# Performance work log

Measured on AMD Instinct MI355X. Metric: run time of the kernel, lower is better.

Reference implementation:

```python
import jax, jax.numpy as jnp
import numpy as np

DIM = 1024
N_HEADS = 16
HEAD_DIM = DIM // N_HEADS
EPS = 1e-05
ROPE_BASE = 1000000.0


def apply_rope(x, base=ROPE_BASE):
    # x: [b, seq, heads, head_dim]
    b, seq, n_heads, dim = x.shape
    half = dim // 2
    i = jnp.arange(half)
    theta = 1.0 / base ** (2 * i / dim)
    pos = jnp.arange(seq)
    angles = pos[:, None] * theta[None, :]            # [seq, half]
    cos = jnp.cos(angles)[None, :, None, :]           # [1, seq, 1, half]
    sin = jnp.sin(angles)[None, :, None, :]
    x1, x2 = jnp.split(x, 2, axis=-1)
    return jnp.concatenate([x1 * cos - x2 * sin, x1 * sin + x2 * cos], axis=-1)


def setup_inputs() -> dict:
    key = jax.random.key(0)
    ks = jax.random.split(key, 6)
    b, seq = 2, 2048
    scale = 1.0 / np.sqrt(DIM)
    x = jax.random.normal(ks[0], (b, seq, DIM), dtype=jnp.float32)
    w_norm = jnp.ones((DIM,), dtype=jnp.float32)
    Wq = jax.random.normal(ks[1], (DIM, DIM), dtype=jnp.float32) * scale
    Wk = jax.random.normal(ks[2], (DIM, DIM), dtype=jnp.float32) * scale
    Wv = jax.random.normal(ks[3], (DIM, DIM), dtype=jnp.float32) * scale
    Wo = jax.random.normal(ks[4], (DIM, DIM), dtype=jnp.float32) * scale
    return {"x": x, "w_norm": w_norm, "Wq": Wq, "Wk": Wk, "Wv": Wv, "Wo": Wo}


def reference(x, w_norm, Wq, Wk, Wv, Wo):
    b, seq, d = x.shape
    # RMSNorm
    rms = jnp.sqrt(jnp.mean(x * x, axis=-1, keepdims=True) + EPS)
    x_norm = x / rms * w_norm
    # QKV projections (Dense without bias: y = x @ W)
    q = (x_norm @ Wq).reshape(b, seq, N_HEADS, HEAD_DIM)
    k = (x_norm @ Wk).reshape(b, seq, N_HEADS, HEAD_DIM)
    v = (x_norm @ Wv).reshape(b, seq, N_HEADS, HEAD_DIM)
    q = apply_rope(q)
    k = apply_rope(k)
    # Causal attention with full [b,h,t,s] scores (faithful to source)
    scores = jnp.einsum('bthd,bshd->bhts', q, k) / jnp.sqrt(jnp.float32(HEAD_DIM))
    causal = jnp.triu(jnp.full((seq, seq), -jnp.inf, dtype=scores.dtype), k=1)
    scores = scores + causal[None, None, :, :]
    attn = jax.nn.softmax(scores, axis=-1)
    out = jnp.einsum('bhts,bshd->bthd', attn, v).reshape(b, seq, d)
    return out @ Wo
```

## Files before the change

kernel.cpp:

```cpp
#include <hip/hip_runtime.h>

#define DIM 1024
#define SEQ 2048
#define BATCH 2
#define NHEADS 16
#define HD 64
#define ROWS (BATCH * SEQ)

typedef __bf16 bf16x8 __attribute__((ext_vector_type(8)));
typedef __bf16 bf16x4 __attribute__((ext_vector_type(4)));
typedef float f32x4 __attribute__((ext_vector_type(4)));

__device__ __forceinline__ f32x4 f4zero() {
    f32x4 z = {0.f, 0.f, 0.f, 0.f};
    return z;
}

#define GLOAD_LDS16(g, l)                                                                  \
    __builtin_amdgcn_global_load_lds((const __attribute__((address_space(1))) void*)(g),   \
                                     (__attribute__((address_space(3))) void*)(l), 16, 0, 0)

__global__ __launch_bounds__(256) void rmsnorm_bf16(const float* __restrict__ x,
                                                    const float* __restrict__ w,
                                                    __bf16* __restrict__ xn) {
    int row = blockIdx.x;
    int t = threadIdx.x;
    float4 v = ((const float4*)(x + (size_t)row * DIM))[t];
    float ss = v.x * v.x + v.y * v.y + v.z * v.z + v.w * v.w;
#pragma unroll
    for (int off = 1; off < 64; off <<= 1) ss += __shfl_xor(ss, off);
    __shared__ float red[4];
    if ((t & 63) == 0) red[t >> 6] = ss;
    __syncthreads();
    ss = red[0] + red[1] + red[2] + red[3];
    float scale = rsqrtf(ss * (1.0f / DIM) + 1e-5f);
    float4 wv = ((const float4*)w)[t];
    bf16x4 o;
    o[0] = (__bf16)(v.x * scale * wv.x);
    o[1] = (__bf16)(v.y * scale * wv.y);
    o[2] = (__bf16)(v.z * scale * wv.z);
    o[3] = (__bf16)(v.w * scale * wv.w);
    *(bf16x4*)(xn + (size_t)row * DIM + t * 4) = o;
}

__global__ __launch_bounds__(256) void wcvt_kernel(const float* __restrict__ Wq,
                                                   const float* __restrict__ Wk,
                                                   const float* __restrict__ Wv,
                                                   const float* __restrict__ Wo,
                                                   __bf16* tq, __bf16* tk, __bf16* tv, __bf16* to_) {
    int z = blockIdx.z;
    const float* W = z == 0 ? Wq : z == 1 ? Wk : z == 2 ? Wv : Wo;
    __bf16* T = z == 0 ? tq : z == 1 ? tk : z == 2 ? tv : to_;
    __shared__ float tile[32][33];
    int n0 = blockIdx.x * 32, k0 = blockIdx.y * 32;
    int tx = threadIdx.x & 31, ty = threadIdx.x >> 5;
#pragma unroll
    for (int j = 0; j < 32; j += 8) tile[ty + j][tx] = W[(size_t)(k0 + ty + j) * DIM + n0 + tx];
    __syncthreads();
#pragma unroll
    for (int j = 0; j < 32; j += 8)
        T[(size_t)(n0 + ty + j) * DIM + k0 + tx] = (__bf16)tile[tx][ty + j];
}

__global__ __launch_bounds__(256) void rope_table_kernel(float* __restrict__ cosT,
                                                         float* __restrict__ sinT) {
    int idx = blockIdx.x * 256 + threadIdx.x;
    int s = idx >> 5, i = idx & 31;
    float e = (2.0f * (float)i) / 64.0f;
    float theta = 1.0f / powf(1000000.0f, e);
    float ang = (float)s * theta;
    cosT[idx] = cosf(ang);
    sinT[idx] = sinf(ang);
}

__global__ __launch_bounds__(256) void rope_apply_bf16(__bf16* __restrict__ q,
                                                       __bf16* __restrict__ k,
                                                       const float* __restrict__ cosT,
                                                       const float* __restrict__ sinT) {
    int idx = blockIdx.x * 256 + threadIdx.x;
    __bf16* t = blockIdx.y ? k : q;
    int row = idx >> 6, rem = idx & 63;
    int head = rem >> 2, i0 = (rem & 3) * 8;
    int s = row & (SEQ - 1);
    size_t base = (size_t)row * DIM + head * HD + i0;
    bf16x8 x1 = *(const bf16x8*)&t[base];
    bf16x8 x2 = *(const bf16x8*)&t[base + 32];
    const float* cp = cosT + s * 32 + i0;
    const float* sp = sinT + s * 32 + i0;
    bf16x8 y1, y2;
#pragma unroll
    for (int j = 0; j < 8; ++j) {
        float a = (float)x1[j], b = (float)x2[j];
        float c = cp[j], sn = sp[j];
        y1[j] = (__bf16)(a * c - b * sn);
        y2[j] = (__bf16)(a * sn + b * c);
    }
    *(bf16x8*)&t[base] = y1;
    *(bf16x8*)&t[base + 32] = y2;
}

__global__ __launch_bounds__(256) void vtrans_kernel(const __bf16* __restrict__ v,
                                                     __bf16* __restrict__ vt) {
    __shared__ __bf16 tile[32][33];
    int bh = blockIdx.z;
    int b = bh >> 4, h = bh & 15;
    int s0 = blockIdx.x * 32, d0 = blockIdx.y * 32;
    int tx = threadIdx.x & 31, ty = threadIdx.x >> 5;
    const __bf16* src = v + (size_t)(b * SEQ) * DIM + h * HD;
#pragma unroll
    for (int j = 0; j < 32; j += 8) tile[ty + j][tx] = src[(size_t)(s0 + ty + j) * DIM + d0 + tx];
    __syncthreads();
    __bf16* dst = vt + ((size_t)bh * HD + d0) * SEQ + s0;
#pragma unroll
    for (int j = 0; j < 32; j += 8) dst[(size_t)(ty + j) * SEQ + tx] = tile[tx][ty + j];
}

template <typename OutT>
__device__ __forceinline__ void gemm_body(const __bf16* __restrict__ A,
                                          const __bf16* __restrict__ Bt,
                                          OutT* __restrict__ C,
                                          int K, int N, int row0, int col0) {
    __shared__ __bf16 As[128 * 32];
    __shared__ __bf16 Bs[128 * 32];
    int tid = threadIdx.x;
    int w = tid >> 6, l = tid & 63, l15 = l & 15, g = l >> 4;
    int wr = (w >> 1) << 6, wc = (w & 1) << 6;

    int sr0 = tid >> 2;
    int sr1 = 64 + (tid >> 2);
    int lc0 = (((tid & 3) ^ ((tid >> 3) & 3)) << 3);
    const __bf16* gA0 = A + (size_t)(row0 + sr0) * K + lc0;
    const __bf16* gA1 = A + (size_t)(row0 + sr1) * K + lc0;
    const __bf16* gB0 = Bt + (size_t)(col0 + sr0) * K + lc0;
    const __bf16* gB1 = Bt + (size_t)(col0 + sr1) * K + lc0;
    __bf16* lA0 = As + w * 512;
    __bf16* lA1 = As + 2048 + w * 512;
    __bf16* lB0 = Bs + w * 512;
    __bf16* lB1 = Bs + 2048 + w * 512;

    int rca = ((g ^ ((l15 >> 1) & 3)) << 3);

    f32x4 acc[4][4];
#pragma unroll
    for (int i = 0; i < 4; ++i)
#pragma unroll
        for (int j = 0; j < 4; ++j) acc[i][j] = f4zero();

    for (int k0 = 0; k0 < K; k0 += 32) {
        __syncthreads();
        GLOAD_LDS16(gA0 + k0, lA0);
        GLOAD_LDS16(gA1 + k0, lA1);
        GLOAD_LDS16(gB0 + k0, lB0);
        GLOAD_LDS16(gB1 + k0, lB1);
        __syncthreads();

        bf16x8 af[4], bfr[4];
#pragma unroll
        for (int i = 0; i < 4; ++i) af[i] = *(const bf16x8*)&As[(wr + i * 16 + l15) * 32 + rca];
#pragma unroll
        for (int j = 0; j < 4; ++j) bfr[j] = *(const bf16x8*)&Bs[(wc + j * 16 + l15) * 32 + rca];
        __builtin_amdgcn_s_setprio(1);
#pragma unroll
        for (int i = 0; i < 4; ++i)
#pragma unroll
            for (int j = 0; j < 4; ++j)
                acc[i][j] = __builtin_amdgcn_mfma_f32_16x16x32_bf16(af[i], bfr[j], acc[i][j], 0, 0, 0);
        __builtin_amdgcn_s_setprio(0);
    }
#pragma unroll
    for (int i = 0; i < 4; ++i)
#pragma unroll
        for (int j = 0; j < 4; ++j)
#pragma unroll
            for (int r = 0; r < 4; ++r) {
                int row = row0 + wr + i * 16 + g * 4 + r;
                int col = col0 + wc + j * 16 + l15;
                C[(size_t)row * N + col] = (OutT)acc[i][j][r];
            }
}

__global__ __launch_bounds__(256) void gemm_qkv_kernel(const __bf16* __restrict__ xn,
                                                       const __bf16* __restrict__ wq,
                                                       const __bf16* __restrict__ wk,
                                                       const __bf16* __restrict__ wv,
                                                       __bf16* q, __bf16* k, __bf16* v) {
    int z = blockIdx.z;
    const __bf16* Bt = z == 0 ? wq : z == 1 ? wk : wv;
    __bf16* C = z == 0 ? q : z == 1 ? k : v;
    gemm_body<__bf16>(xn, Bt, C, DIM, DIM, (int)blockIdx.y << 7, (int)blockIdx.x << 7);
}

__global__ __launch_bounds__(256) void gemm_out_kernel(const __bf16* __restrict__ ctx,
                                                       const __bf16* __restrict__ wo,
                                                       float* __restrict__ out) {
    gemm_body<float>(ctx, wo, out, DIM, DIM, (int)blockIdx.y << 7, (int)blockIdx.x << 7);
}

__global__ __launch_bounds__(256) void attn_mfma_kernel(const __bf16* __restrict__ q,
                                                        const __bf16* __restrict__ k,
                                                        const __bf16* __restrict__ vt,
                                                        __bf16* __restrict__ ctx) {
    int bh = blockIdx.x;
    int qt = 31 - (int)blockIdx.y;
    int b = bh >> 4, h = bh & 15;
    int q0 = qt << 6;
    __shared__ __bf16 Ks[128][72];
    __shared__ __bf16 Vl[64][136];
    __shared__ __bf16 Ps[4][16][136];
    int tid = threadIdx.x, w = tid >> 6, l = tid & 63, l15 = l & 15, g = l >> 4;
    size_t hoff = (size_t)(b * SEQ) * DIM + h * HD;
    const __bf16* vth = vt + (size_t)bh * HD * SEQ;

    bf16x8 aq[2];
    {
        int qrow = q0 + w * 16 + l15;
        bf16x8 t0 = *(const bf16x8*)&q[hoff + (size_t)qrow * DIM + g * 8];
        bf16x8 t1 = *(const bf16x8*)&q[hoff + (size_t)qrow * DIM + 32 + g * 8];
        const float c2 = 0.125f * 1.44269504f;
#pragma unroll
        for (int j = 0; j < 8; ++j) {
            aq[0][j] = (__bf16)((float)t0[j] * c2);
            aq[1][j] = (__bf16)((float)t1[j] * c2);
        }
    }

    f32x4 acc_o[4];
#pragma unroll
    for (int j = 0; j < 4; ++j) acc_o[j] = f4zero();
    float m_run[4], l_run[4];
#pragma unroll
    for (int r = 0; r < 4; ++r) {
        m_run[r] = -1e30f;
        l_run[r] = 0.f;
    }

    int ksr = tid >> 3, kd0 = (tid & 7) * 8;
    int vdr = tid >> 4, vs0 = (tid & 15) * 8;

    int nst = (q0 + 191) >> 7;
    bf16x8 rk[4], rv[4];
#pragma unroll
    for (int c = 0; c < 4; ++c) {
        rk[c] = *(const bf16x8*)&k[hoff + (size_t)(c * 32 + ksr) * DIM + kd0];
        rv[c] = *(const bf16x8*)&vth[(size_t)(c * 16 + vdr) * SEQ + vs0];
    }

    for (int st = 0; st < nst; ++st) {
        int s0 = st << 7;
        __syncthreads();
#pragma unroll
        for (int c = 0; c < 4; ++c) {
            *(bf16x8*)&Ks[c * 32 + ksr][kd0] = rk[c];
            *(bf16x8*)&Vl[c * 16 + vdr][vs0] = rv[c];
        }
        __syncthreads();
        if (st + 1 < nst) {
            int sn = s0 + 128;
#pragma unroll
            for (int c = 0; c < 4; ++c) {
                rk[c] = *(const bf16x8*)&k[hoff + (size_t)(sn + c * 32 + ksr) * DIM + kd0];
                rv[c] = *(const bf16x8*)&vth[(size_t)(c * 16 + vdr) * SEQ + sn + vs0];
            }
        }

        f32x4 sacc[8];
#pragma unroll
        for (int j = 0; j < 8; ++j) sacc[j] = f4zero();
        __builtin_amdgcn_s_setprio(1);
#pragma unroll
        for (int j = 0; j < 8; ++j) {
            bf16x8 bk0 = *(const bf16x8*)&Ks[j * 16 + l15][g * 8];
            bf16x8 bk1 = *(const bf16x8*)&Ks[j * 16 + l15][32 + g * 8];
            sacc[j] = __builtin_amdgcn_mfma_f32_16x16x32_bf16(aq[0], bk0, sacc[j], 0, 0, 0);
            sacc[j] = __builtin_amdgcn_mfma_f32_16x16x32_bf16(aq[1], bk1, sacc[j], 0, 0, 0);
        }
        __builtin_amdgcn_s_setprio(0);

        if (st == nst - 1) {
#pragma unroll
            for (int j = 0; j < 8; ++j) {
                int scol = s0 + j * 16 + l15;
#pragma unroll
                for (int r = 0; r < 4; ++r) {
                    int rowq = q0 + w * 16 + g * 4 + r;
                    if (scol > rowq) sacc[j][r] = -1e30f;
                }
            }
        }

#pragma unroll
        for (int r = 0; r < 4; ++r) {
            float tl = sacc[0][r];
#pragma unroll
            for (int j = 1; j < 8; ++j) tl = fmaxf(tl, sacc[j][r]);
            if (!__all(tl <= m_run[r] + 11.0f)) {
#pragma unroll
                for (int off = 1; off < 16; off <<= 1) tl = fmaxf(tl, __shfl_xor(tl, off));
                float m_new = fmaxf(m_run[r], tl);
                float alpha = exp2f(m_run[r] - m_new);
                l_run[r] *= alpha;
#pragma unroll
                for (int jd = 0; jd < 4; ++jd) acc_o[jd][r] *= alpha;
                m_run[r] = m_new;
            }
            float rs = 0.f;
#pragma unroll
            for (int j = 0; j < 8; ++j) {
                float p = exp2f(sacc[j][r] - m_run[r]);
                Ps[w][g * 4 + r][j * 16 + l15] = (__bf16)p;
                rs += p;
            }
#pragma unroll
            for (int off = 1; off < 16; off <<= 1) rs += __shfl_xor(rs, off);
            l_run[r] += rs;
        }

        bf16x8 ap[4];
#pragma unroll
        for (int ks = 0; ks < 4; ++ks) ap[ks] = *(const bf16x8*)&Ps[w][l15][ks * 32 + g * 8];
        __builtin_amdgcn_s_setprio(1);
#pragma unroll
        for (int jd = 0; jd < 4; ++jd)
#pragma unroll
            for (int ks = 0; ks < 4; ++ks) {
                bf16x8 bv = *(const bf16x8*)&Vl[jd * 16 + l15][ks * 32 + g * 8];
                acc_o[jd] = __builtin_amdgcn_mfma_f32_16x16x32_bf16(ap[ks], bv, acc_o[jd], 0, 0, 0);
            }
        __builtin_amdgcn_s_setprio(0);
    }

#pragma unroll
    for (int r = 0; r < 4; ++r) {
        float inv = 1.0f / l_run[r];
        int row = q0 + w * 16 + g * 4 + r;
#pragma unroll
        for (int jd = 0; jd < 4; ++jd)
            ctx[hoff + (size_t)row * DIM + jd * 16 + l15] = (__bf16)(acc_o[jd][r] * inv);
    }
}

extern "C" void kernel_launch(void* const* d_in, const int* in_sizes, int n_in,
                              void* d_out, int out_size, void* d_ws, size_t ws_size,
                              hipStream_t stream) {
    const float* x = (const float*)d_in[0];
    const float* w_norm = (const float*)d_in[1];
    const float* Wq = (const float*)d_in[2];
    const float* Wk = (const float*)d_in[3];
    const float* Wv = (const float*)d_in[4];
    const float* Wo = (const float*)d_in[5];
    float* out = (float*)d_out;
    char* w8 = (char*)d_ws;

    __bf16* xn = (__bf16*)(w8);
    __bf16* wtq = (__bf16*)(w8 + (8ull << 20));
    __bf16* wtk = (__bf16*)(w8 + (10ull << 20));
    __bf16* wtv = (__bf16*)(w8 + (12ull << 20));
    __bf16* wto = (__bf16*)(w8 + (14ull << 20));
    __bf16* qb = (__bf16*)(w8 + (16ull << 20));
    __bf16* kb = (__bf16*)(w8 + (24ull << 20));
    __bf16* vb = (__bf16*)(w8 + (32ull << 20));
    __bf16* vtb = (__bf16*)(w8 + (40ull << 20));
    __bf16* ctx = (__bf16*)(w8 + (48ull << 20));
    float* cosT = (float*)(w8 + (56ull << 20));
    float* sinT = cosT + SEQ * 32;

    wcvt_kernel<<<dim3(32, 32, 4), 256, 0, stream>>>(Wq, Wk, Wv, Wo, wtq, wtk, wtv, wto);
    rmsnorm_bf16<<<ROWS, 256, 0, stream>>>(x, w_norm, xn);
    rope_table_kernel<<<(SEQ * 32) / 256, 256, 0, stream>>>(cosT, sinT);

    gemm_qkv_kernel<<<dim3(DIM / 128, ROWS / 128, 3), 256, 0, stream>>>(xn, wtq, wtk, wtv, qb, kb, vb);

    rope_apply_bf16<<<dim3((ROWS * 64) / 256, 2), 256, 0, stream>>>(qb, kb, cosT, sinT);
    vtrans_kernel<<<dim3(SEQ / 32, HD / 32, BATCH * NHEADS), 256, 0, stream>>>(vb, vtb);

    attn_mfma_kernel<<<dim3(BATCH * NHEADS, SEQ / 64), 256, 0, stream>>>(qb, kb, vtb, ctx);

    gemm_out_kernel<<<dim3(DIM / 128, ROWS / 128), 256, 0, stream>>>(ctx, wto, out);
}
```

Before: 149.5 us.

## Fuse RoPE and V-transpose into QKV GEMM epilogue; rewrite attention with 32x32 MFMA

Applies RoPE in the QKV GEMM epilogue and writes V directly in transposed layout, which removes the separate rope_apply and vtrans kernels along with their global round trips. The attention kernel is rewritten to use 32x32x16 MFMA with 128-query blocks and 64-key tiles. It computes S^T so probabilities stay in registers, repacked with cvt_pk and permlane32_swap instead of going through LDS. The risks are higher register pressure from the two 16-wide accumulators and fewer workgroups in the attention grid.

```diff
diff --git a/kernel.cpp b/kernel.cpp
--- a/kernel.cpp
+++ b/kernel.cpp
@@ -10,10 +10,22 @@
 typedef __bf16 bf16x8 __attribute__((ext_vector_type(8)));
 typedef __bf16 bf16x4 __attribute__((ext_vector_type(4)));
 typedef float f32x4 __attribute__((ext_vector_type(4)));
+typedef float f32x16 __attribute__((ext_vector_type(16)));
+typedef unsigned u32x4 __attribute__((ext_vector_type(4)));
 
 __device__ __forceinline__ f32x4 f4zero() {
     f32x4 z = {0.f, 0.f, 0.f, 0.f};
     return z;
+}
+
+__device__ __forceinline__ unsigned cvtpk(float lo, float hi) {
+    unsigned r;
+    asm("v_cvt_pk_bf16_f32 %0, %1, %2" : "=v"(r) : "v"(lo), "v"(hi));
+    return r;
+}
+
+__device__ __forceinline__ void pl32swap(unsigned& a, unsigned& b) {
+    asm volatile("v_permlane32_swap_b32 %0, %1" : "+v"(a), "+v"(b));
 }
 
 #define GLOAD_LDS16(g, l)                                                                  \
@@ -73,55 +85,10 @@
     sinT[idx] = sinf(ang);
 }
 
-__global__ __launch_bounds__(256) void rope_apply_bf16(__bf16* __restrict__ q,
-                                                       __bf16* __restrict__ k,
-                                                       const float* __restrict__ cosT,
-                                                       const float* __restrict__ sinT) {
-    int idx = blockIdx.x * 256 + threadIdx.x;
-    __bf16* t = blockIdx.y ? k : q;
-    int row = idx >> 6, rem = idx & 63;
-    int head = rem >> 2, i0 = (rem & 3) * 8;
-    int s = row & (SEQ - 1);
-    size_t base = (size_t)row * DIM + head * HD + i0;
-    bf16x8 x1 = *(const bf16x8*)&t[base];
-    bf16x8 x2 = *(const bf16x8*)&t[base + 32];
-    const float* cp = cosT + s * 32 + i0;
-    const float* sp = sinT + s * 32 + i0;
-    bf16x8 y1, y2;
-#pragma unroll
-    for (int j = 0; j < 8; ++j) {
-        float a = (float)x1[j], b = (float)x2[j];
-        float c = cp[j], sn = sp[j];
-        y1[j] = (__bf16)(a * c - b * sn);
-        y2[j] = (__bf16)(a * sn + b * c);
-    }
-    *(bf16x8*)&t[base] = y1;
-    *(bf16x8*)&t[base + 32] = y2;
-}
-
-__global__ __launch_bounds__(256) void vtrans_kernel(const __bf16* __restrict__ v,
-                                                     __bf16* __restrict__ vt) {
-    __shared__ __bf16 tile[32][33];
-    int bh = blockIdx.z;
-    int b = bh >> 4, h = bh & 15;
-    int s0 = blockIdx.x * 32, d0 = blockIdx.y * 32;
-    int tx = threadIdx.x & 31, ty = threadIdx.x >> 5;
-    const __bf16* src = v + (size_t)(b * SEQ) * DIM + h * HD;
-#pragma unroll
-    for (int j = 0; j < 32; j += 8) tile[ty + j][tx] = src[(size_t)(s0 + ty + j) * DIM + d0 + tx];
-    __syncthreads();
-    __bf16* dst = vt + ((size_t)bh * HD + d0) * SEQ + s0;
-#pragma unroll
-    for (int j = 0; j < 32; j += 8) dst[(size_t)(ty + j) * SEQ + tx] = tile[tx][ty + j];
-}
-
-template <typename OutT>
-__device__ __forceinline__ void gemm_body(const __bf16* __restrict__ A,
+__device__ __forceinline__ void gemm_core(const __bf16* __restrict__ A,
                                           const __bf16* __restrict__ Bt,
-                                          OutT* __restrict__ C,
-                                          int K, int N, int row0, int col0) {
-    __shared__ __bf16 As[128 * 32];
-    __shared__ __bf16 Bs[128 * 32];
+                                          int K, __bf16* As, __bf16* Bs,
+                                          f32x4 (&acc)[4][4], int row0, int col0) {
     int tid = threadIdx.x;
     int w = tid >> 6, l = tid & 63, l15 = l & 15, g = l >> 4;
     int wr = (w >> 1) << 6, wc = (w & 1) << 6;
@@ -140,7 +107,6 @@
 
     int rca = ((g ^ ((l15 >> 1) & 3)) << 3);
 
-    f32x4 acc[4][4];
 #pragma unroll
     for (int i = 0; i < 4; ++i)
 #pragma unroll
@@ -167,33 +133,86 @@
                 acc[i][j] = __builtin_amdgcn_mfma_f32_16x16x32_bf16(af[i], bfr[j], acc[i][j], 0, 0, 0);
         __builtin_amdgcn_s_setprio(0);
     }
-#pragma unroll
-    for (int i = 0; i < 4; ++i)
-#pragma unroll
-        for (int j = 0; j < 4; ++j)
-#pragma unroll
-            for (int r = 0; r < 4; ++r) {
-                int row = row0 + wr + i * 16 + g * 4 + r;
-                int col = col0 + wc + j * 16 + l15;
-                C[(size_t)row * N + col] = (OutT)acc[i][j][r];
-            }
 }
 
 __global__ __launch_bounds__(256) void gemm_qkv_kernel(const __bf16* __restrict__ xn,
                                                        const __bf16* __restrict__ wq,
                                                        const __bf16* __restrict__ wk,
                                                        const __bf16* __restrict__ wv,
-                                                       __bf16* q, __bf16* k, __bf16* v) {
+                                                       __bf16* __restrict__ qo,
+                                                       __bf16* __restrict__ ko,
+                                                       __bf16* __restrict__ vt,
+                                                       const float* __restrict__ cosT,
+                                                       const float* __restrict__ sinT) {
+    __shared__ __bf16 As[128 * 32];
+    __shared__ __bf16 Bs[128 * 32];
     int z = blockIdx.z;
     const __bf16* Bt = z == 0 ? wq : z == 1 ? wk : wv;
-    __bf16* C = z == 0 ? q : z == 1 ? k : v;
-    gemm_body<__bf16>(xn, Bt, C, DIM, DIM, (int)blockIdx.y << 7, (int)blockIdx.x << 7);
+    int row0 = (int)blockIdx.y << 7, col0 = (int)blockIdx.x << 7;
+    f32x4 acc[4][4];
+    gemm_core(xn, Bt, DIM, As, Bs, acc, row0, col0);
+
+    int tid = threadIdx.x;
+    int w = tid >> 6, l = tid & 63, l15 = l & 15, g = l >> 4;
+    int wr = (w >> 1) << 6, wc = (w & 1) << 6;
+    int colbase = col0 + wc;
+
+    if (z == 2) {
+        int bh = ((row0 >> 11) << 4) + (colbase >> 6);
+#pragma unroll
+        for (int i = 0; i < 4; ++i) {
+            int sbase = (row0 + wr + i * 16 + g * 4) & (SEQ - 1);
+#pragma unroll
+            for (int j = 0; j < 4; ++j) {
+                int d = j * 16 + l15;
+                bf16x4 o;
+#pragma unroll
+                for (int r = 0; r < 4; ++r) o[r] = (__bf16)acc[i][j][r];
+                *(bf16x4*)&vt[((size_t)bh * HD + d) * SEQ + sbase] = o;
+            }
+        }
+    } else {
+        __bf16* C = z == 0 ? qo : ko;
+#pragma unroll
+        for (int i = 0; i < 4; ++i) {
+#pragma unroll
+            for (int r = 0; r < 4; ++r) {
+                int row = row0 + wr + i * 16 + g * 4 + r;
+                int s = row & (SEQ - 1);
+#pragma unroll
+                for (int j = 0; j < 2; ++j) {
+                    float c = cosT[s * 32 + j * 16 + l15];
+                    float sn = sinT[s * 32 + j * 16 + l15];
+                    float x1 = acc[i][j][r], x2 = acc[i][j + 2][r];
+                    C[(size_t)row * DIM + colbase + j * 16 + l15] = (__bf16)(x1 * c - x2 * sn);
+                    C[(size_t)row * DIM + colbase + (j + 2) * 16 + l15] = (__bf16)(x1 * sn + x2 * c);
+                }
+            }
+        }
+    }
 }
 
 __global__ __launch_bounds__(256) void gemm_out_kernel(const __bf16* __restrict__ ctx,
                                                        const __bf16* __restrict__ wo,
                                                        float* __restrict__ out) {
-    gemm_body<float>(ctx, wo, out, DIM, DIM, (int)blockIdx.y << 7, (int)blockIdx.x << 7);
+    __shared__ __bf16 As[128 * 32];
+    __shared__ __bf16 Bs[128 * 32];
+    int row0 = (int)blockIdx.y << 7, col0 = (int)blockIdx.x << 7;
+    f32x4 acc[4][4];
+    gemm_core(ctx, wo, DIM, As, Bs, acc, row0, col0);
+    int tid = threadIdx.x;
+    int w = tid >> 6, l = tid & 63, l15 = l & 15, g = l >> 4;
+    int wr = (w >> 1) << 6, wc = (w & 1) << 6;
+#pragma unroll
+    for (int i = 0; i < 4; ++i)
+#pragma unroll
+        for (int j = 0; j < 4; ++j)
+#pragma unroll
+            for (int r = 0; r < 4; ++r) {
+                int row = row0 + wr + i * 16 + g * 4 + r;
+                int col = col0 + wc + j * 16 + l15;
+                out[(size_t)row * DIM + col] = acc[i][j][r];
+            }
 }
 
 __global__ __launch_bounds__(256) void attn_mfma_kernel(const __bf16* __restrict__ q,
@@ -201,141 +220,153 @@
                                                         const __bf16* __restrict__ vt,
                                                         __bf16* __restrict__ ctx) {
     int bh = blockIdx.x;
-    int qt = 31 - (int)blockIdx.y;
+    int qb = 15 - (int)blockIdx.y;
     int b = bh >> 4, h = bh & 15;
-    int q0 = qt << 6;
-    __shared__ __bf16 Ks[128][72];
-    __shared__ __bf16 Vl[64][136];
-    __shared__ __bf16 Ps[4][16][136];
-    int tid = threadIdx.x, w = tid >> 6, l = tid & 63, l15 = l & 15, g = l >> 4;
+    __shared__ __bf16 Ks[64][72];
+    __shared__ __bf16 Vs[64][72];
+    int tid = threadIdx.x, w = tid >> 6, l = tid & 63;
+    int l31 = l & 31, hi = l >> 5;
     size_t hoff = (size_t)(b * SEQ) * DIM + h * HD;
     const __bf16* vth = vt + (size_t)bh * HD * SEQ;
-
-    bf16x8 aq[2];
-    {
-        int qrow = q0 + w * 16 + l15;
-        bf16x8 t0 = *(const bf16x8*)&q[hoff + (size_t)qrow * DIM + g * 8];
-        bf16x8 t1 = *(const bf16x8*)&q[hoff + (size_t)qrow * DIM + 32 + g * 8];
-        const float c2 = 0.125f * 1.44269504f;
-#pragma unroll
-        for (int j = 0; j < 8; ++j) {
-            aq[0][j] = (__bf16)((float)t0[j] * c2);
-            aq[1][j] = (__bf16)((float)t1[j] * c2);
-        }
-    }
-
-    f32x4 acc_o[4];
-#pragma unroll
-    for (int j = 0; j < 4; ++j) acc_o[j] = f4zero();
-    float m_run[4], l_run[4];
-#pragma unroll
-    for (int r = 0; r < 4; ++r) {
-        m_run[r] = -1e30f;
-        l_run[r] = 0.f;
-    }
-
-    int ksr = tid >> 3, kd0 = (tid & 7) * 8;
-    int vdr = tid >> 4, vs0 = (tid & 15) * 8;
-
-    int nst = (q0 + 191) >> 7;
-    bf16x8 rk[4], rv[4];
-#pragma unroll
-    for (int c = 0; c < 4; ++c) {
-        rk[c] = *(const bf16x8*)&k[hoff + (size_t)(c * 32 + ksr) * DIM + kd0];
-        rv[c] = *(const bf16x8*)&vth[(size_t)(c * 16 + vdr) * SEQ + vs0];
-    }
+    int qw0 = qb * 128 + w * 32;
+    int qrow = qw0 + l31;
+    int qmax = qw0 + 31;
+    int nst = 2 * qb + 2;
+
+    bf16x8 qf[4];
+    const float c2 = 0.125f * 1.44269504f;
+#pragma unroll
+    for (int g = 0; g < 4; ++g) {
+        bf16x8 t0 = *(const bf16x8*)&q[hoff + (size_t)qrow * DIM + g * 16 + hi * 8];
+#pragma unroll
+        for (int e = 0; e < 8; ++e) qf[g][e] = (__bf16)((float)t0[e] * c2);
+    }
+
+    f32x16 oA, oB;
+#pragma unroll
+    for (int r = 0; r < 16; ++r) {
+        oA[r] = 0.f;
+        oB[r] = 0.f;
+    }
+    float m_run = -1e30f, l_run = 0.f;
+
+    int sr = tid >> 3, sc = (tid & 7) * 8;
+    bf16x8 rk0, rk1, rv0, rv1;
+    rk0 = *(const bf16x8*)&k[hoff + (size_t)sr * DIM + sc];
+    rk1 = *(const bf16x8*)&k[hoff + (size_t)(32 + sr) * DIM + sc];
+    rv0 = *(const bf16x8*)&vth[(size_t)sr * SEQ + sc];
+    rv1 = *(const bf16x8*)&vth[(size_t)(32 + sr) * SEQ + sc];
 
     for (int st = 0; st < nst; ++st) {
-        int s0 = st << 7;
+        int s0 = st << 6;
         __syncthreads();
-#pragma unroll
-        for (int c = 0; c < 4; ++c) {
-            *(bf16x8*)&Ks[c * 32 + ksr][kd0] = rk[c];
-            *(bf16x8*)&Vl[c * 16 + vdr][vs0] = rv[c];
-        }
+        *(bf16x8*)&Ks[sr][sc] = rk0;
+        *(bf16x8*)&Ks[32 + sr][sc] = rk1;
+        *(bf16x8*)&Vs[sr][sc] = rv0;
+        *(bf16x8*)&Vs[32 + sr][sc] = rv1;
         __syncthreads();
         if (st + 1 < nst) {
-            int sn = s0 + 128;
-#pragma unroll
-            for (int c = 0; c < 4; ++c) {
-                rk[c] = *(const bf16x8*)&k[hoff + (size_t)(sn + c * 32 + ksr) * DIM + kd0];
-                rv[c] = *(const bf16x8*)&vth[(size_t)(c * 16 + vdr) * SEQ + sn + vs0];
+            int sn = s0 + 64;
+            rk0 = *(const bf16x8*)&k[hoff + (size_t)(sn + sr) * DIM + sc];
+            rk1 = *(const bf16x8*)&k[hoff + (size_t)(sn + 32 + sr) * DIM + sc];
+            rv0 = *(const bf16x8*)&vth[(size_t)sr * SEQ + sn + sc];
+            rv1 = *(const bf16x8*)&vth[(size_t)(32 + sr) * SEQ + sn + sc];
+        }
+        if (s0 > qmax) continue;
+
+        f32x16 sa, sb;
+#pragma unroll
+        for (int r = 0; r < 16; ++r) {
+            sa[r] = 0.f;
+            sb[r] = 0.f;
+        }
+        __builtin_amdgcn_s_setprio(1);
+#pragma unroll
+        for (int g = 0; g < 4; ++g) {
+            bf16x8 ka = *(const bf16x8*)&Ks[l31][g * 16 + hi * 8];
+            bf16x8 kb2 = *(const bf16x8*)&Ks[32 + l31][g * 16 + hi * 8];
+            sa = __builtin_amdgcn_mfma_f32_32x32x16_bf16(ka, qf[g], sa, 0, 0, 0);
+            sb = __builtin_amdgcn_mfma_f32_32x32x16_bf16(kb2, qf[g], sb, 0, 0, 0);
+        }
+        __builtin_amdgcn_s_setprio(0);
+
+        if (s0 + 63 > qw0) {
+#pragma unroll
+            for (int r = 0; r < 16; ++r) {
+                int kg = s0 + (r & 3) + 8 * (r >> 2) + 4 * hi;
+                if (kg > qrow) sa[r] = -1e30f;
+                if (kg + 32 > qrow) sb[r] = -1e30f;
             }
         }
 
-        f32x4 sacc[8];
-#pragma unroll
-        for (int j = 0; j < 8; ++j) sacc[j] = f4zero();
+        float lmax = -3e38f;
+#pragma unroll
+        for (int r = 0; r < 16; ++r) lmax = fmaxf(lmax, fmaxf(sa[r], sb[r]));
+        if (!__all(lmax <= m_run + 10.0f)) {
+            float omax = fmaxf(lmax, __shfl_xor(lmax, 32));
+            float m_new = fmaxf(m_run, omax);
+            float alpha = exp2f(m_run - m_new);
+            l_run *= alpha;
+#pragma unroll
+            for (int r = 0; r < 16; ++r) {
+                oA[r] *= alpha;
+                oB[r] *= alpha;
+            }
+            m_run = m_new;
+        }
+        float ls = 0.f;
+#pragma unroll
+        for (int r = 0; r < 16; ++r) {
+            sa[r] = exp2f(sa[r] - m_run);
+            ls += sa[r];
+            sb[r] = exp2f(sb[r] - m_run);
+            ls += sb[r];
+        }
+        l_run += ls + __shfl_xor(ls, 32);
+
+        bf16x8 pa[4];
+#pragma unroll
+        for (int g = 0; g < 2; ++g) {
+            unsigned a_ = cvtpk(sa[8 * g + 0], sa[8 * g + 1]);
+            unsigned b_ = cvtpk(sa[8 * g + 4], sa[8 * g + 5]);
+            pl32swap(a_, b_);
+            unsigned c_ = cvtpk(sa[8 * g + 2], sa[8 * g + 3]);
+            unsigned d_ = cvtpk(sa[8 * g + 6], sa[8 * g + 7]);
+            pl32swap(c_, d_);
+            u32x4 t4 = {a_, c_, b_, d_};
+            pa[g] = __builtin_bit_cast(bf16x8, t4);
+        }
+#pragma unroll
+        for (int g = 0; g < 2; ++g) {
+            unsigned a_ = cvtpk(sb[8 * g + 0], sb[8 * g + 1]);
+            unsigned b_ = cvtpk(sb[8 * g + 4], sb[8 * g + 5]);
+            pl32swap(a_, b_);
+            unsigned c_ = cvtpk(sb[8 * g + 2], sb[8 * g + 3]);
+            unsigned d_ = cvtpk(sb[8 * g + 6], sb[8 * g + 7]);
+            pl32swap(c_, d_);
+            u32x4 t4 = {a_, c_, b_, d_};
+            pa[2 + g] = __builtin_bit_cast(bf16x8, t4);
+        }
+
         __builtin_amdgcn_s_setprio(1);
 #pragma unroll
-        for (int j = 0; j < 8; ++j) {
-            bf16x8 bk0 = *(const bf16x8*)&Ks[j * 16 + l15][g * 8];
-            bf16x8 bk1 = *(const bf16x8*)&Ks[j * 16 + l15][32 + g * 8];
-            sacc[j] = __builtin_amdgcn_mfma_f32_16x16x32_bf16(aq[0], bk0, sacc[j], 0, 0, 0);
-            sacc[j] = __builtin_amdgcn_mfma_f32_16x16x32_bf16(aq[1], bk1, sacc[j], 0, 0, 0);
+        for (int ks = 0; ks < 4; ++ks) {
+            bf16x8 va = *(const bf16x8*)&Vs[l31][ks * 16 + hi * 8];
+            bf16x8 vb2 = *(const bf16x8*)&Vs[32 + l31][ks * 16 + hi * 8];
+            oA = __builtin_amdgcn_mfma_f32_32x32x16_bf16(va, pa[ks], oA, 0, 0, 0);
+            oB = __builtin_amdgcn_mfma_f32_32x32x16_bf16(vb2, pa[ks], oB, 0, 0, 0);
         }
         __builtin_amdgcn_s_setprio(0);
-
-        if (st == nst - 1) {
-#pragma unroll
-            for (int j = 0; j < 8; ++j) {
-                int scol = s0 + j * 16 + l15;
-#pragma unroll
-                for (int r = 0; r < 4; ++r) {
-                    int rowq = q0 + w * 16 + g * 4 + r;
-                    if (scol > rowq) sacc[j][r] = -1e30f;
-                }
-            }
-        }
-
-#pragma unroll
-        for (int r = 0; r < 4; ++r) {
-            float tl = sacc[0][r];
-#pragma unroll
-            for (int j = 1; j < 8; ++j) tl = fmaxf(tl, sacc[j][r]);
-            if (!__all(tl <= m_run[r] + 11.0f)) {
-#pragma unroll
-                for (int off = 1; off < 16; off <<= 1) tl = fmaxf(tl, __shfl_xor(tl, off));
-                float m_new = fmaxf(m_run[r], tl);
-                float alpha = exp2f(m_run[r] - m_new);
-                l_run[r] *= alpha;
-#pragma unroll
-                for (int jd = 0; jd < 4; ++jd) acc_o[jd][r] *= alpha;
-                m_run[r] = m_new;
-            }
-            float rs = 0.f;
-#pragma unroll
-            for (int j = 0; j < 8; ++j) {
-                float p = exp2f(sacc[j][r] - m_run[r]);
-                Ps[w][g * 4 + r][j * 16 + l15] = (__bf16)p;
-                rs += p;
-            }
-#pragma unroll
-            for (int off = 1; off < 16; off <<= 1) rs += __shfl_xor(rs, off);
-            l_run[r] += rs;
-        }
-
-        bf16x8 ap[4];
-#pragma unroll
-        for (int ks = 0; ks < 4; ++ks) ap[ks] = *(const bf16x8*)&Ps[w][l15][ks * 32 + g * 8];
-        __builtin_amdgcn_s_setprio(1);
-#pragma unroll
-        for (int jd = 0; jd < 4; ++jd)
-#pragma unroll
-            for (int ks = 0; ks < 4; ++ks) {
-                bf16x8 bv = *(const bf16x8*)&Vl[jd * 16 + l15][ks * 32 + g * 8];
-                acc_o[jd] = __builtin_amdgcn_mfma_f32_16x16x32_bf16(ap[ks], bv, acc_o[jd], 0, 0, 0);
-            }
-        __builtin_amdgcn_s_setprio(0);
-    }
-
-#pragma unroll
-    for (int r = 0; r < 4; ++r) {
-        float inv = 1.0f / l_run[r];
-        int row = q0 + w * 16 + g * 4 + r;
-#pragma unroll
-        for (int jd = 0; jd < 4; ++jd)
-            ctx[hoff + (size_t)row * DIM + jd * 16 + l15] = (__bf16)(acc_o[jd][r] * inv);
+    }
+
+    float inv = 1.0f / l_run;
+#pragma unroll
+    for (int r = 0; r < 16; r += 2) {
+        int d = (r & 3) + 8 * (r >> 2) + 4 * hi;
+        unsigned pA = cvtpk(oA[r] * inv, oA[r + 1] * inv);
+        unsigned pB = cvtpk(oB[r] * inv, oB[r + 1] * inv);
+        *(unsigned*)&ctx[hoff + (size_t)qrow * DIM + d] = pA;
+        *(unsigned*)&ctx[hoff + (size_t)qrow * DIM + 32 + d] = pB;
     }
 }
 
@@ -358,22 +389,19 @@
     __bf16* wto = (__bf16*)(w8 + (14ull << 20));
     __bf16* qb = (__bf16*)(w8 + (16ull << 20));
     __bf16* kb = (__bf16*)(w8 + (24ull << 20));
-    __bf16* vb = (__bf16*)(w8 + (32ull << 20));
-    __bf16* vtb = (__bf16*)(w8 + (40ull << 20));
-    __bf16* ctx = (__bf16*)(w8 + (48ull << 20));
-    float* cosT = (float*)(w8 + (56ull << 20));
+    __bf16* vtb = (__bf16*)(w8 + (32ull << 20));
+    __bf16* ctx = (__bf16*)(w8 + (40ull << 20));
+    float* cosT = (float*)(w8 + (48ull << 20));
     float* sinT = cosT + SEQ * 32;
 
     wcvt_kernel<<<dim3(32, 32, 4), 256, 0, stream>>>(Wq, Wk, Wv, Wo, wtq, wtk, wtv, wto);
     rmsnorm_bf16<<<ROWS, 256, 0, stream>>>(x, w_norm, xn);
     rope_table_kernel<<<(SEQ * 32) / 256, 256, 0, stream>>>(cosT, sinT);
 
-    gemm_qkv_kernel<<<dim3(DIM / 128, ROWS / 128, 3), 256, 0, stream>>>(xn, wtq, wtk, wtv, qb, kb, vb);
-
-    rope_apply_bf16<<<dim3((ROWS * 64) / 256, 2), 256, 0, stream>>>(qb, kb, cosT, sinT);
-    vtrans_kernel<<<dim3(SEQ / 32, HD / 32, BATCH * NHEADS), 256, 0, stream>>>(vb, vtb);
-
-    attn_mfma_kernel<<<dim3(BATCH * NHEADS, SEQ / 64), 256, 0, stream>>>(qb, kb, vtb, ctx);
+    gemm_qkv_kernel<<<dim3(DIM / 128, ROWS / 128, 3), 256, 0, stream>>>(
+        xn, wtq, wtk, wtv, qb, kb, vtb, cosT, sinT);
+
+    attn_mfma_kernel<<<dim3(BATCH * NHEADS, SEQ / 128), 256, 0, stream>>>(qb, kb, vtb, ctx);
 
     gemm_out_kernel<<<dim3(DIM / 128, ROWS / 128), 256, 0, stream>>>(ctx, wto, out);
 }
```

Result: no change. 150.8 us (+0.8%).
